# Kernel optimization log

Hardware: AMD Instinct MI355X
Metric: run time of the kernel (lower is better)

Reference implementation:

```python
import jax, jax.numpy as jnp
import numpy as np
from jax import lax

KERNEL = 3
NUM_ITERS = 10
SMOOTH = 1.0


def _max_pool3d(x):
    # x: (B, 1, Z, Y, X); 3x3x3 max pool, stride 1, SAME padding
    return lax.reduce_window(
        x, -jnp.inf, lax.max,
        window_dimensions=(1, 1, KERNEL, KERNEL, KERNEL),
        window_strides=(1, 1, 1, 1, 1),
        padding='SAME')


def _soft_erode(x):
    return -_max_pool3d(-x)


def _soft_dilate(x):
    return _max_pool3d(x)


def _soft_open(x):
    return _soft_dilate(_soft_erode(x))


def _soft_skeletonize(img):
    skel = jax.nn.relu(img - _soft_open(img))
    for _ in range(NUM_ITERS):
        img = _soft_erode(img)
        delta = jax.nn.relu(img - _soft_open(img))
        skel = skel + jax.nn.relu(delta - skel * delta)
    return skel


def setup_inputs() -> dict:
    key = jax.random.key(0)
    k1, k2 = jax.random.split(key)
    B, C, Z, Y, X = 2, 2, 192, 192, 192
    logits = jax.random.normal(k1, (B, C, Z, Y, X), dtype=jnp.float32)
    targets = jax.random.randint(k2, (B, Z, Y, X), 0, 2, dtype=jnp.int32)
    return {"logits": logits, "targets": targets}


def reference(logits, targets):
    probs = jax.nn.softmax(logits, axis=1)
    pred_surface = probs[:, 1:2]                                  # (B,1,Z,Y,X)
    gt_surface = (targets == 1).astype(jnp.float32)[:, None]      # (B,1,Z,Y,X)
    skel_pred = _soft_skeletonize(pred_surface)
    skel_gt = _soft_skeletonize(gt_surface)
    tprec = (jnp.sum(skel_pred * gt_surface) + SMOOTH) / (jnp.sum(skel_pred) + SMOOTH)
    tsens = (jnp.sum(skel_gt * pred_surface) + SMOOTH) / (jnp.sum(skel_gt) + SMOOTH)
    cl_dice = 2.0 * tprec * tsens / (tprec + tsens + 1e-07)
    return 1.0 - cl_dice
```

## Files before the change

kernel.cpp:

```cpp
#include <hip/hip_runtime.h>
#include <hip/hip_fp16.h>


#define ZD 192
#define YD 192
#define XD 192
constexpr int PLANE = YD * XD;
constexpr int VOL   = ZD * PLANE;
constexpr int NVOL4 = 4 * VOL;

constexpr int XT = 64, YT = 16, ZCH = 16;

constexpr int AWQ = 18, SA_Q = 19, AH = 22;
constexpr int NAQ = AH * AWQ;
constexpr int EWQ = 17, SE_Q = 17;
constexpr int E1H = 20;
constexpr int NE1Q = E1H * EWQ;
constexpr int E2H = 18;
constexpr int NE2Q = E2H * EWQ;
constexpr int F2STEPS = ZCH + 8;
constexpr int SAW2 = SA_Q * 2;
constexpr int SEW2 = SE_Q * 2;

constexpr int IWQ = 18, SIW = 19;
constexpr int IH  = 20;
constexpr int NIMGQ = IH * IWQ;
constexpr int BWQ = 17, BH = 18;
constexpr int NBQ  = BH * BWQ;
constexpr int TSTEPS = ZCH + 4;
#define PINF __builtin_inff()

typedef _Float16 hv2 __attribute__((ext_vector_type(2)));
struct __align__(8) H4 { hv2 lo, hi; };

__device__ __forceinline__ unsigned h2u(hv2 h) { return __builtin_bit_cast(unsigned, h); }
__device__ __forceinline__ hv2 u2h(unsigned u) { return __builtin_bit_cast(hv2, u); }

__device__ __forceinline__ hv2 h2min(hv2 a, hv2 b) {
#if __has_builtin(__builtin_elementwise_min)
    return __builtin_elementwise_min(a, b);
#else
    unsigned r, ua = h2u(a), ub = h2u(b);
    asm("v_pk_min_f16 %0, %1, %2" : "=v"(r) : "v"(ua), "v"(ub));
    return u2h(r);
#endif
}
__device__ __forceinline__ hv2 h2max(hv2 a, hv2 b) {
#if __has_builtin(__builtin_elementwise_max)
    return __builtin_elementwise_max(a, b);
#else
    unsigned r, ua = h2u(a), ub = h2u(b);
    asm("v_pk_max_f16 %0, %1, %2" : "=v"(r) : "v"(ua), "v"(ub));
    return u2h(r);
#endif
}
__device__ __forceinline__ hv2 shf1(hv2 c, hv2 n) {
    return u2h(__builtin_amdgcn_alignbit(h2u(n), h2u(c), 16));
}
__device__ __forceinline__ H4 h4min(H4 a, H4 b) { H4 r; r.lo = h2min(a.lo, b.lo); r.hi = h2min(a.hi, b.hi); return r; }
__device__ __forceinline__ H4 h4max(H4 a, H4 b) { H4 r; r.lo = h2max(a.lo, b.lo); r.hi = h2max(a.hi, b.hi); return r; }
__device__ __forceinline__ H4 pk4(float4 v) {
    H4 r;
    r.lo.x = (_Float16)v.x; r.lo.y = (_Float16)v.y;
    r.hi.x = (_Float16)v.z; r.hi.y = (_Float16)v.w;
    return r;
}
__device__ __forceinline__ H4 ldp4(const __half* p) {
    const uint2 v = *(const uint2*)p;
    H4 r; r.lo = u2h(v.x); r.hi = u2h(v.y); return r;
}
__device__ __forceinline__ void stp4(__half* p, H4 v) {
    uint2 u; u.x = h2u(v.lo); u.y = h2u(v.hi);
    *(uint2*)p = u;
}
__device__ __forceinline__ void sth4(__half* p, float4 v) { stp4(p, pk4(v)); }

template <int MODE>
__global__ __launch_bounds__(256)
void fused2p_kernel(const __half* __restrict__ a_in,
                    __half* __restrict__ a_out,
                    __half* __restrict__ skel,
                    const float* __restrict__ logits,
                    const int* __restrict__ targets)
{
    __shared__ __align__(16) hv2 sA [AH  * SA_Q * 2];
    __shared__ __align__(16) hv2 sE1[E1H * SE_Q * 2 + 2];
    __shared__ __align__(16) hv2 sE2[E2H * SE_Q * 2];

    const int tx = threadIdx.x, ty = threadIdx.y;
    const int tid = ty * 16 + tx;
    const int x0 = (blockIdx.x % 3) * XT, y0 = (blockIdx.x / 3) * YT;
    const int z0 = blockIdx.y * ZCH;
    const int zf = blockIdx.z;
    const int bb = zf & 1, field = zf >> 1;
    const size_t voff = (size_t)zf * VOL;
    const __half* inb  = a_in  + voff;
    __half*       outb = a_out + voff;
    __half*       skb  = skel  + voff;
    const float* lg0 = logits + (size_t)(bb * 2) * VOL;
    const float* lg1 = lg0 + VOL;
    const int*   tgb = targets + (size_t)bb * VOL;

    const hv2 INF2  = u2h(0x7C007C00u);
    const hv2 NINF2 = u2h(0xFC00FC00u);
    const hv2 Z2    = u2h(0u);
    const H4 HINF4  = { INF2, INF2 };
    const H4 HNINF4 = { NINF2, NINF2 };
    const H4 HZ4    = { Z2, Z2 };
    const _Float16 HN1 = (_Float16)(-PINF);

    const int q1off = ((tid & 3) << 6) + (tid >> 2);

    int a_ad[2], a_go[2]; bool a_ok[2], a_h[2];
    #pragma unroll
    for (int j = 0; j < 2; ++j) {
        const int qi = (j == 0) ? tid : 256 + q1off;
        const int r = qi / AWQ, c = qi - r * AWQ;
        const int gy = y0 - 3 + r, gxb = x0 - 4 + 4 * c;
        a_h[j]  = (qi < NAQ);
        a_ok[j] = a_h[j] && gy >= 0 && gy < YD && gxb >= 0 && gxb < XD;
        a_go[j] = gy * XD + gxb;
        a_ad[j] = (r * SA_Q + c) * 2;
    }
    int e1st[2], e1rd[2]; bool e1h[2]; H4 e1m[2];
    #pragma unroll
    for (int j = 0; j < 2; ++j) {
        const int qi = (j == 0) ? tid : 256 + q1off;
        const int r = qi / EWQ, c = qi - r * EWQ;
        e1h[j]  = (qi < NE1Q);
        e1st[j] = (r * SE_Q + c) * 2;
        e1rd[j] = (r * SA_Q + c) * 2;
        const int gy = y0 - 2 + r, gxb = x0 - 2 + 4 * c;
        const bool yv = (gy >= 0 && gy < YD);
        float4 m;
        m.x = (yv && gxb     >= 0 && gxb     < XD) ? -PINF : PINF;
        m.y = (yv && gxb + 1 >= 0 && gxb + 1 < XD) ? -PINF : PINF;
        m.z = (yv && gxb + 2 >= 0 && gxb + 2 < XD) ? -PINF : PINF;
        m.w = (yv && gxb + 3 >= 0 && gxb + 3 < XD) ? -PINF : PINF;
        e1m[j] = pk4(m);
    }
    int e2st[2], e2rd[2]; bool e2h[2]; H4 e2m[2];
    #pragma unroll
    for (int j = 0; j < 2; ++j) {
        const int qi = (j == 0) ? tid : 256 + q1off;
        const int r = qi / EWQ, c = qi - r * EWQ;
        e2h[j]  = (qi < NE2Q);
        e2st[j] = (r * SE_Q + c) * 2;
        e2rd[j] = (r * SE_Q + c) * 2;
        const int gy = y0 - 1 + r, gxb = x0 - 1 + 4 * c;
        const bool yv = (gy >= 0 && gy < YD);
        float4 m;
        m.x = (yv && gxb     >= 0 && gxb     < XD) ? PINF : -PINF;
        m.y = (yv && gxb + 1 >= 0 && gxb + 1 < XD) ? PINF : -PINF;
        m.z = (yv && gxb + 2 >= 0 && gxb + 2 < XD) ? PINF : -PINF;
        m.w = (yv && gxb + 3 >= 0 && gxb + 3 < XD) ? PINF : -PINF;
        e2m[j] = pk4(m);
    }

    const int gy0 = y0 + ty, gx0 = x0 + 4 * tx;
    const bool rok0 = (gy0 > 0), rok2 = (gy0 < YD - 1);
    const bool lok  = (gx0 > 0), rokx = (gx0 + 4 < XD);

    auto loadq = [&](int zi, int j) -> H4 {
        if (zi < 0 || zi >= ZD || zi > z0 + ZCH + 2 || !a_ok[j]) return HINF4;
        const size_t p = (size_t)zi * PLANE + a_go[j];
        if constexpr (MODE == 0) {
            if (field) {
                const int4 t = *(const int4*)(tgb + p);
                return pk4(make_float4(t.x == 1 ? 1.f : 0.f, t.y == 1 ? 1.f : 0.f,
                                       t.z == 1 ? 1.f : 0.f, t.w == 1 ? 1.f : 0.f));
            } else {
                const float4 a = *(const float4*)(lg0 + p);
                const float4 b = *(const float4*)(lg1 + p);
                return pk4(make_float4(1.f / (1.f + __expf(a.x - b.x)),
                                       1.f / (1.f + __expf(a.y - b.y)),
                                       1.f / (1.f + __expf(a.z - b.z)),
                                       1.f / (1.f + __expf(a.w - b.w))));
            }
        } else {
            return ldp4(inb + p);
        }
    };

    auto s1p = [&](int j) -> H4 {
        const hv2* p = sA + e1rd[j];
        const H4 A0 = *(const H4*)p;
        const H4 B0 = *(const H4*)(p + 2);
        const H4 A1 = *(const H4*)(p + SAW2);
        const H4 B1 = *(const H4*)(p + SAW2 + 2);
        const H4 A2 = *(const H4*)(p + 2 * SAW2);
        const H4 B2 = *(const H4*)(p + 2 * SAW2 + 2);
        const hv2 Al = h2min(A0.lo, h2min(A1.lo, A2.lo));
        const hv2 Ah = h2min(A0.hi, h2min(A1.hi, A2.hi));
        const hv2 Bl = h2min(B0.lo, h2min(B1.lo, B2.lo));
        const hv2 Bh = h2min(B0.hi, h2min(B1.hi, B2.hi));
        const hv2 M1 = shf1(Al, Ah);
        const hv2 M2 = shf1(Ah, Bl);
        const hv2 M3 = shf1(Bl, Bh);
        H4 r;
        r.lo = h2min(M1, h2min(Ah, M2));
        r.hi = h2min(M2, h2min(Bl, M3));
        return r;
    };
    auto s2p = [&](int j) -> H4 {
        const hv2* p = sE1 + e2rd[j];
        const H4 E0 = *(const H4*)p;
        const hv2 F0 = p[2];
        const H4 E1 = *(const H4*)(p + SEW2);
        const hv2 F1 = p[SEW2 + 2];
        const H4 E2 = *(const H4*)(p + 2 * SEW2);
        const hv2 F2 = p[2 * SEW2 + 2];
        const hv2 El = h2min(E0.lo, h2min(E1.lo, E2.lo));
        const hv2 Eh = h2min(E0.hi, h2min(E1.hi, E2.hi));
        const hv2 Fl = h2min(F0, h2min(F1, F2));
        const hv2 M1 = shf1(El, Eh);
        const hv2 M2 = shf1(Eh, Fl);
        H4 r;
        r.lo = h2min(El, h2min(M1, Eh));
        r.hi = h2min(Eh, h2min(M2, Fl));
        return r;
    };

    H4 s1p2a = HINF4, s1p1a = HINF4, s1p2b = HINF4, s1p1b = HINF4;
    H4 s2p2a = HINF4, s2p1a = HINF4, s2p2b = HINF4, s2p1b = HINF4;
    H4 xm1p2 = HNINF4, xm1p1 = HNINF4;
    H4 xm2p2 = HNINF4, xm2p1 = HNINF4;
    H4 e1w0 = HINF4, e1w1 = HINF4, e2w0 = HINF4, e2w1 = HINF4;
    H4 icp1 = HZ4, icp2 = HZ4, icp3 = HZ4;
    H4 ec1 = HZ4, ec2 = HZ4, ec3 = HZ4;
    H4 e2cp = HZ4;
    H4 dl1r1 = HZ4, dl1r2 = HZ4;

    const size_t eb = (size_t)gy0 * XD + gx0;

    H4 ca0 = loadq(z0 - 3, 0);
    H4 ca1 = loadq(z0 - 3, 1);

    #pragma unroll 1
    for (int s = 0; s < F2STEPS; ++s) {
        const int z = z0 - 3 + s;
        *(H4*)&sA[a_ad[0]] = ca0;
        if (a_h[1]) *(H4*)&sA[a_ad[1]] = ca1;
        if (s >= 1) {
            *(H4*)&sE1[e1st[0]] = h4max(e1w0, e1m[0]);
            if (e1h[1]) *(H4*)&sE1[e1st[1]] = h4max(e1w1, e1m[1]);
        }
        if (s >= 2) {
            *(H4*)&sE2[e2st[0]] = h4min(e2w0, e2m[0]);
            if (e2h[1]) *(H4*)&sE2[e2st[1]] = h4min(e2w1, e2m[1]);
        }
        __syncthreads();

        if (s + 1 < F2STEPS) { ca0 = loadq(z + 1, 0); ca1 = loadq(z + 1, 1); }

        {
            const H4 cur = s1p(0);
            e1w0 = h4min(s1p2a, h4min(s1p1a, cur));
            s1p2a = s1p1a; s1p1a = cur;
        }
        if (e1h[1]) {
            const H4 cur = s1p(1);
            e1w1 = h4min(s1p2b, h4min(s1p1b, cur));
            s1p2b = s1p1b; s1p1b = cur;
        }

        const int  ze1 = z - 2;
        const bool ve1 = (s >= 1) && (ze1 >= 0) && (ze1 < ZD);

        {
            const H4 cur = ve1 ? s2p(0) : HINF4;
            e2w0 = h4min(s2p2a, h4min(s2p1a, cur));
            s2p2a = s2p1a; s2p1a = cur;
        }
        if (e2h[1]) {
            const H4 cur = ve1 ? s2p(1) : HINF4;
            e2w1 = h4min(s2p2b, h4min(s2p1b, cur));
            s2p2b = s2p1b; s2p1b = cur;
        }

        H4 xm1c = HNINF4, e1cc = HZ4;
        if (ve1) {
            const hv2* p = sE1 + ((ty + 1) * SE_Q + tx) * 2;
            H4 A0 = *(const H4*)p;
            H4 Bq0 = *(const H4*)(p + 2);
            const H4 A1 = *(const H4*)(p + SEW2);
            const H4 Bq1 = *(const H4*)(p + SEW2 + 2);
            H4 A2 = *(const H4*)(p + 2 * SEW2);
            H4 Bq2 = *(const H4*)(p + 2 * SEW2 + 2);
            e1cc.lo = A1.hi;
            e1cc.hi = Bq1.lo;
            if (!rok0) { A0 = HNINF4; Bq0 = HNINF4; }
            if (!rok2) { A2 = HNINF4; Bq2 = HNINF4; }
            const hv2 Al = h2max(A0.lo, h2max(A1.lo, A2.lo));
            const hv2 Ah = h2max(A0.hi, h2max(A1.hi, A2.hi));
            const hv2 Bl = h2max(Bq0.lo, h2max(Bq1.lo, Bq2.lo));
            const hv2 Bh = h2max(Bq0.hi, h2max(Bq1.hi, Bq2.hi));
            hv2 M1 = shf1(Al, Ah);
            const hv2 M2 = shf1(Ah, Bl);
            hv2 M3 = shf1(Bl, Bh);
            if (!lok)  M1.x = HN1;
            if (!rokx) M3.y = HN1;
            xm1c.lo = h2max(M1, h2max(Ah, M2));
            xm1c.hi = h2max(M2, h2max(Bl, M3));
        }
        const H4 d1v = h4max(xm1p2, h4max(xm1p1, xm1c));
        xm1p2 = xm1p1; xm1p1 = xm1c;

        const int  ze2 = z - 4;
        const bool ve2 = (s >= 2) && (ze2 >= 0) && (ze2 < ZD);
        H4 xm2c = HNINF4, e2cc = HZ4;
        if (ve2) {
            const hv2* p = sE2 + (ty * SE_Q + tx) * 2;
            const H4 U0 = *(const H4*)p;
            const hv2 V0 = p[2];
            const H4 U1 = *(const H4*)(p + SEW2);
            const hv2 V1 = p[SEW2 + 2];
            const H4 U2 = *(const H4*)(p + 2 * SEW2);
            const hv2 V2 = p[2 * SEW2 + 2];
            e2cc.lo = shf1(U1.lo, U1.hi);
            e2cc.hi = shf1(U1.hi, V1);
            const hv2 Ul = h2max(U0.lo, h2max(U1.lo, U2.lo));
            const hv2 Uh = h2max(U0.hi, h2max(U1.hi, U2.hi));
            const hv2 Vl = h2max(V0, h2max(V1, V2));
            const hv2 M1 = shf1(Ul, Uh);
            const hv2 M2 = shf1(Uh, Vl);
            xm2c.lo = h2max(Ul, h2max(M1, Uh));
            xm2c.hi = h2max(Uh, h2max(M2, Vl));
        }
        const H4 d2v = h4max(xm2p2, h4max(xm2p1, xm2c));
        xm2p2 = xm2p1; xm2p1 = xm2c;

        const H4 icq = *(const H4*)&sA[((ty + 3) * SA_Q + tx + 1) * 2];

        float4 dl1n, dl2;
        dl1n.x = fmaxf((float)icp3.lo.x - (float)d1v.lo.x, 0.f);
        dl1n.y = fmaxf((float)icp3.lo.y - (float)d1v.lo.y, 0.f);
        dl1n.z = fmaxf((float)icp3.hi.x - (float)d1v.hi.x, 0.f);
        dl1n.w = fmaxf((float)icp3.hi.y - (float)d1v.hi.y, 0.f);
        dl2.x = fmaxf((float)ec3.lo.x - (float)d2v.lo.x, 0.f);
        dl2.y = fmaxf((float)ec3.lo.y - (float)d2v.lo.y, 0.f);
        dl2.z = fmaxf((float)ec3.hi.x - (float)d2v.hi.x, 0.f);
        dl2.w = fmaxf((float)ec3.hi.y - (float)d2v.hi.y, 0.f);
        const H4 dA = dl1r2;
        const H4 av = e2cp;

        __syncthreads();

        if (s >= 8) {
            const int zo = z - 5;
            const size_t idx = (size_t)zo * PLANE + eb;
            float4 sk;
            const float dAx = (float)dA.lo.x, dAy = (float)dA.lo.y;
            const float dAz = (float)dA.hi.x, dAw = (float)dA.hi.y;
            if constexpr (MODE == 0) {
                sk = make_float4(dAx, dAy, dAz, dAw);
            } else {
                const H4 s0 = ldp4(skb + idx);
                const float s0x = (float)s0.lo.x, s0y = (float)s0.lo.y;
                const float s0z = (float)s0.hi.x, s0w = (float)s0.hi.y;
                sk.x = s0x + dAx * (1.f - s0x);
                sk.y = s0y + dAy * (1.f - s0y);
                sk.z = s0z + dAz * (1.f - s0z);
                sk.w = s0w + dAw * (1.f - s0w);
            }
            float4 sv;
            sv.x = sk.x + dl2.x * (1.f - sk.x);
            sv.y = sk.y + dl2.y * (1.f - sk.y);
            sv.z = sk.z + dl2.z * (1.f - sk.z);
            sv.w = sk.w + dl2.w * (1.f - sk.w);
            sth4(skb + idx, sv);
            stp4(outb + idx, av);
        }

        dl1r2 = dl1r1; dl1r1 = pk4(dl1n);
        icp3 = icp2; icp2 = icp1; icp1 = icq;
        ec3 = ec2; ec2 = ec1; ec1 = e1cc;
        e2cp = e2cc;
    }
}

template <int MODE>
__global__ __launch_bounds__(256)
void fused_kernel(const __half* __restrict__ a_in,
                  __half* __restrict__ a_out,
                  __half* __restrict__ skel,
                  const float* __restrict__ logits,
                  const int* __restrict__ targets,
                  float* __restrict__ sums)
{
    __shared__ __align__(16) hv2 simg[2][IH * SIW * 2];
    __shared__ __align__(16) hv2 sbp[NBQ * 2 + 4];
    __shared__ float red[4][2];

    const int tx = threadIdx.x, ty = threadIdx.y;
    const int tid = ty * 16 + tx;
    const int x0 = (blockIdx.x % 3) * XT, y0 = (blockIdx.x / 3) * YT;
    const int z0 = blockIdx.y * ZCH;
    const int zf = blockIdx.z;
    const int bb = zf & 1, field = zf >> 1;
    const size_t voff = (size_t)zf * VOL;
    const __half* inb  = a_in  + voff;
    __half*       skb  = skel  + voff;
    const float* lg0 = logits + (size_t)(bb * 2) * VOL;
    const float* lg1 = lg0 + VOL;
    const int*   tgb = targets + (size_t)bb * VOL;

    const hv2 INF2  = u2h(0x7C007C00u);
    const hv2 NINF2 = u2h(0xFC00FC00u);
    const hv2 Z2    = u2h(0u);
    const H4 HINF4  = { INF2, INF2 };
    const H4 HNINF4 = { NINF2, NINF2 };
    const H4 HZ4    = { Z2, Z2 };

    const int q1off = ((tid & 3) << 6) + (tid >> 2);

    int im_qi[2] = { tid, 256 + q1off };
    int im_addr[2], im_goff[2]; bool im_ok[2], im_has[2];
    #pragma unroll
    for (int j = 0; j < 2; ++j) {
        const int qi = im_qi[j];
        const int r = qi / IWQ, c = qi - r * IWQ;
        const int gy = y0 - 2 + r, gxb = x0 - 4 + 4 * c;
        im_has[j] = (qi < NIMGQ);
        im_ok[j]  = im_has[j] && gy >= 0 && gy < YD && gxb >= 0 && gxb < XD;
        im_goff[j] = gy * XD + gxb;
        im_addr[j] = (r * SIW + c) * 2;
    }
    int bqi[2], brow[2], bcol[2]; bool bhas[2]; H4 bmask[2];
    #pragma unroll
    for (int j = 0; j < 2; ++j) {
        const int qi = (j == 0) ? tid : 256 + q1off;
        bqi[j] = qi;
        bhas[j] = (qi < NBQ);
        const int r = qi / BWQ, c = qi - r * BWQ;
        brow[j] = r; bcol[j] = c;
        const int gy = y0 - 1 + r, gxb = x0 - 1 + 4 * c;
        const bool yv = (gy >= 0 && gy < YD);
        float4 m;
        m.x = (yv && gxb     >= 0 && gxb     < XD) ? PINF : -PINF;
        m.y = (yv && gxb + 1 >= 0 && gxb + 1 < XD) ? PINF : -PINF;
        m.z = (yv && gxb + 2 >= 0 && gxb + 2 < XD) ? PINF : -PINF;
        m.w = (yv && gxb + 3 >= 0 && gxb + 3 < XD) ? PINF : -PINF;
        bmask[j] = pk4(m);
    }

    auto loadq = [&](int zi, int j) -> H4 {
        if (zi < 0 || zi >= ZD || !im_ok[j]) return HINF4;
        const size_t p = (size_t)zi * PLANE + im_goff[j];
        return ldp4(inb + p);
    };

    auto s1_of = [&](const hv2* sp, int j) -> H4 {
        const hv2* p = sp + (brow[j] * SIW + bcol[j]) * 2;
        const hv2 A0 = p[1];
        const hv2 A1 = p[SIW * 2 + 1];
        const hv2 A2 = p[SIW * 4 + 1];
        const H4 B0 = *(const H4*)(p + 2);
        const H4 B1 = *(const H4*)(p + SIW * 2 + 2);
        const H4 B2 = *(const H4*)(p + SIW * 4 + 2);
        const hv2 Ah = h2min(A0, h2min(A1, A2));
        const hv2 Bl = h2min(B0.lo, h2min(B1.lo, B2.lo));
        const hv2 Bh = h2min(B0.hi, h2min(B1.hi, B2.hi));
        const hv2 S1 = shf1(Ah, Bl);
        const hv2 S2 = shf1(Bl, Bh);
        H4 r;
        r.lo = h2min(Ah, h2min(S1, Bl));
        r.hi = h2min(Bl, h2min(S2, Bh));
        return r;
    };

    H4 p2a = HINF4, p1a = HINF4;
    H4 p2b = HINF4, p1b = HINF4;
    H4 s2p1 = HNINF4, s2p2 = HNINF4;
    H4 icp1 = HZ4, icp2 = HZ4;
    float sd = 0.f, ss = 0.f;

    H4 ca0 = loadq(z0 - 2, 0);
    H4 ca1 = loadq(z0 - 2, 1);

    #pragma unroll 2
    for (int s = 0; s < TSTEPS; ++s) {
        const int zi = z0 - 2 + s;
        hv2* sp = simg[s & 1];
        *(H4*)&sp[im_addr[0]] = ca0;
        if (im_has[1]) *(H4*)&sp[im_addr[1]] = ca1;
        if (s + 1 < TSTEPS) { ca0 = loadq(zi + 1, 0); ca1 = loadq(zi + 1, 1); }
        __syncthreads();
        const int zb = zi - 1;
        const bool zbv = (s >= 2) && (zb >= 0) && (zb < ZD);
        {
            const H4 cur = s1_of(sp, 0);
            if (zbv) {
                const H4 b = h4min(h4min(p2a, p1a), cur);
                *(H4*)&sbp[2 * bqi[0]] = h4min(b, bmask[0]);
            }
            p2a = p1a; p1a = cur;
        }
        if (bhas[1]) {
            const H4 cur = s1_of(sp, 1);
            if (zbv) {
                const H4 b = h4min(h4min(p2b, p1b), cur);
                *(H4*)&sbp[2 * bqi[1]] = h4min(b, bmask[1]);
            }
            p2b = p1b; p1b = cur;
        }
        const H4 icq = *(const H4*)&sp[((ty + 2) * SIW + tx + 1) * 2];
        __syncthreads();
        H4 s2n = HNINF4;
        if (zbv) {
            const hv2* p = sbp + (ty * BWQ + tx) * 2;
            const H4 U0 = *(const H4*)p;
            const H4 U1 = *(const H4*)(p + BWQ * 2);
            const H4 U2 = *(const H4*)(p + BWQ * 4);
            const hv2 V0 = p[2];
            const hv2 V1 = p[BWQ * 2 + 2];
            const hv2 V2 = p[BWQ * 4 + 2];
            const hv2 Ul = h2max(U0.lo, h2max(U1.lo, U2.lo));
            const hv2 Uh = h2max(U0.hi, h2max(U1.hi, U2.hi));
            const hv2 Vl = h2max(V0, h2max(V1, V2));
            const hv2 S1 = shf1(Ul, Uh);
            const hv2 S2 = shf1(Uh, Vl);
            s2n.lo = h2max(Ul, h2max(S1, Uh));
            s2n.hi = h2max(Uh, h2max(S2, Vl));
        }
        if (s >= 4) {
            const int zo = zi - 2;
            const H4 d = h4max(s2p2, h4max(s2p1, s2n));
            float4 dl;
            dl.x = fmaxf((float)icp2.lo.x - (float)d.lo.x, 0.f);
            dl.y = fmaxf((float)icp2.lo.y - (float)d.lo.y, 0.f);
            dl.z = fmaxf((float)icp2.hi.x - (float)d.hi.x, 0.f);
            dl.w = fmaxf((float)icp2.hi.y - (float)d.hi.y, 0.f);
            const size_t idx = (size_t)zo * PLANE + (size_t)(y0 + ty) * XD + (x0 + 4 * tx);
            const H4 sk = ldp4(skb + idx);
            const float s0x = (float)sk.lo.x, s0y = (float)sk.lo.y;
            const float s0z = (float)sk.hi.x, s0w = (float)sk.hi.y;
            float4 sv;
            sv.x = s0x + dl.x * (1.f - s0x);
            sv.y = s0y + dl.y * (1.f - s0y);
            sv.z = s0z + dl.z * (1.f - s0z);
            sv.w = s0w + dl.w * (1.f - s0w);
            float4 w;
            if (field) {
                const float4 a = *(const float4*)(lg0 + idx);
                const float4 b = *(const float4*)(lg1 + idx);
                w = make_float4(1.f / (1.f + __expf(a.x - b.x)),
                                1.f / (1.f + __expf(a.y - b.y)),
                                1.f / (1.f + __expf(a.z - b.z)),
                                1.f / (1.f + __expf(a.w - b.w)));
            } else {
                const int4 t = *(const int4*)(tgb + idx);
                w = make_float4(t.x == 1 ? 1.f : 0.f, t.y == 1 ? 1.f : 0.f,
                                t.z == 1 ? 1.f : 0.f, t.w == 1 ? 1.f : 0.f);
            }
            sd += sv.x * w.x + sv.y * w.y + sv.z * w.z + sv.w * w.w;
            ss += sv.x + sv.y + sv.z + sv.w;
        }
        s2p2 = s2p1; s2p1 = s2n;
        icp2 = icp1; icp1 = icq;
    }

    if constexpr (MODE == 2) {
        #pragma unroll
        for (int o = 32; o; o >>= 1) {
            sd += __shfl_down(sd, o, 64);
            ss += __shfl_down(ss, o, 64);
        }
        const int w = tid >> 6;
        if ((tid & 63) == 0) { red[w][0] = sd; red[w][1] = ss; }
        __syncthreads();
        if (tid == 0) {
            float a = 0.f, b = 0.f;
            #pragma unroll
            for (int i = 0; i < 4; ++i) { a += red[i][0]; b += red[i][1]; }
            atomicAdd(&sums[2 * field + 0], a);
            atomicAdd(&sums[2 * field + 1], b);
        }
    }
}

__global__ void final_kernel(const float* __restrict__ sums, float* __restrict__ out)
{
    float tprec = (sums[0] + 1.f) / (sums[1] + 1.f);
    float tsens = (sums[2] + 1.f) / (sums[3] + 1.f);
    float cl = 2.f * tprec * tsens / (tprec + tsens + 1e-7f);
    out[0] = 1.f - cl;
}

extern "C" void kernel_launch(void* const* d_in, const int* in_sizes, int n_in,
                              void* d_out, int out_size, void* d_ws, size_t ws_size,
                              hipStream_t stream)
{
    const float* logits  = (const float*)d_in[0];
    const int*   targets = (const int*)d_in[1];
    float* out  = (float*)d_out;

    float*  sums = (float*)d_ws;
    __half* A    = (__half*)(sums + 16);
    __half* B    = A + NVOL4;
    __half* SK   = B + NVOL4;

    hipMemsetAsync(sums, 0, 16 * sizeof(float), stream);

    dim3 g(3 * (YD / YT), ZD / ZCH, 4);
    dim3 blk(16, 16, 1);

    fused2p_kernel<0><<<g, blk, 0, stream>>>(A, A, SK, logits, targets);
    fused2p_kernel<1><<<g, blk, 0, stream>>>(A, B, SK, logits, targets);
    fused2p_kernel<1><<<g, blk, 0, stream>>>(B, A, SK, logits, targets);
    fused2p_kernel<1><<<g, blk, 0, stream>>>(A, B, SK, logits, targets);
    fused2p_kernel<1><<<g, blk, 0, stream>>>(B, A, SK, logits, targets);
    fused_kernel<2><<<g, blk, 0, stream>>>(A, B, SK, logits, targets, sums);

    final_kernel<<<1, 1, 0, stream>>>(sums, out);
}
```

Baseline: 919.5 us.

## Double-buffer shared plane buffers and drop the second per-step barrier

Gives the sA, sE1 and sE2 shared-memory staging buffers two copies that alternate by step parity. With this, each step writes into one buffer while other threads may still read the previous one, so the trailing __syncthreads per z-step is removed. The loop is also unrolled by two so the buffer selection can become constant. This doubles LDS usage per block, which may lower occupancy, and correctness depends on no reads spanning more than one step.

```diff
diff --git a/kernel.cpp b/kernel.cpp
--- a/kernel.cpp
+++ b/kernel.cpp
@@ -83,9 +83,9 @@
                     const float* __restrict__ logits,
                     const int* __restrict__ targets)
 {
-    __shared__ __align__(16) hv2 sA [AH  * SA_Q * 2];
-    __shared__ __align__(16) hv2 sE1[E1H * SE_Q * 2 + 2];
-    __shared__ __align__(16) hv2 sE2[E2H * SE_Q * 2];
+    __shared__ __align__(16) hv2 sA [2][AH  * SA_Q * 2];
+    __shared__ __align__(16) hv2 sE1[2][E1H * SE_Q * 2 + 2];
+    __shared__ __align__(16) hv2 sE2[2][E2H * SE_Q * 2];
 
     const int tx = threadIdx.x, ty = threadIdx.y;
     const int tid = ty * 16 + tx;
@@ -182,8 +182,8 @@
         }
     };
 
-    auto s1p = [&](int j) -> H4 {
-        const hv2* p = sA + e1rd[j];
+    auto s1p = [&](const hv2* pA, int j) -> H4 {
+        const hv2* p = pA + e1rd[j];
         const H4 A0 = *(const H4*)p;
         const H4 B0 = *(const H4*)(p + 2);
         const H4 A1 = *(const H4*)(p + SAW2);
@@ -202,8 +202,8 @@
         r.hi = h2min(M2, h2min(Bl, M3));
         return r;
     };
-    auto s2p = [&](int j) -> H4 {
-        const hv2* p = sE1 + e2rd[j];
+    auto s2p = [&](const hv2* pE1, int j) -> H4 {
+        const hv2* p = pE1 + e2rd[j];
         const H4 E0 = *(const H4*)p;
         const hv2 F0 = p[2];
         const H4 E1 = *(const H4*)(p + SEW2);
@@ -236,30 +236,33 @@
     H4 ca0 = loadq(z0 - 3, 0);
     H4 ca1 = loadq(z0 - 3, 1);
 
-    #pragma unroll 1
+    #pragma unroll 2
     for (int s = 0; s < F2STEPS; ++s) {
         const int z = z0 - 3 + s;
-        *(H4*)&sA[a_ad[0]] = ca0;
-        if (a_h[1]) *(H4*)&sA[a_ad[1]] = ca1;
+        hv2* pA  = sA [s & 1];
+        hv2* pE1 = sE1[s & 1];
+        hv2* pE2 = sE2[s & 1];
+        *(H4*)&pA[a_ad[0]] = ca0;
+        if (a_h[1]) *(H4*)&pA[a_ad[1]] = ca1;
         if (s >= 1) {
-            *(H4*)&sE1[e1st[0]] = h4max(e1w0, e1m[0]);
-            if (e1h[1]) *(H4*)&sE1[e1st[1]] = h4max(e1w1, e1m[1]);
+            *(H4*)&pE1[e1st[0]] = h4max(e1w0, e1m[0]);
+            if (e1h[1]) *(H4*)&pE1[e1st[1]] = h4max(e1w1, e1m[1]);
         }
         if (s >= 2) {
-            *(H4*)&sE2[e2st[0]] = h4min(e2w0, e2m[0]);
-            if (e2h[1]) *(H4*)&sE2[e2st[1]] = h4min(e2w1, e2m[1]);
+            *(H4*)&pE2[e2st[0]] = h4min(e2w0, e2m[0]);
+            if (e2h[1]) *(H4*)&pE2[e2st[1]] = h4min(e2w1, e2m[1]);
         }
         __syncthreads();
 
         if (s + 1 < F2STEPS) { ca0 = loadq(z + 1, 0); ca1 = loadq(z + 1, 1); }
 
         {
-            const H4 cur = s1p(0);
+            const H4 cur = s1p(pA, 0);
             e1w0 = h4min(s1p2a, h4min(s1p1a, cur));
             s1p2a = s1p1a; s1p1a = cur;
         }
         if (e1h[1]) {
-            const H4 cur = s1p(1);
+            const H4 cur = s1p(pA, 1);
             e1w1 = h4min(s1p2b, h4min(s1p1b, cur));
             s1p2b = s1p1b; s1p1b = cur;
         }
@@ -268,19 +271,19 @@
         const bool ve1 = (s >= 1) && (ze1 >= 0) && (ze1 < ZD);
 
         {
-            const H4 cur = ve1 ? s2p(0) : HINF4;
+            const H4 cur = ve1 ? s2p(pE1, 0) : HINF4;
             e2w0 = h4min(s2p2a, h4min(s2p1a, cur));
             s2p2a = s2p1a; s2p1a = cur;
         }
         if (e2h[1]) {
-            const H4 cur = ve1 ? s2p(1) : HINF4;
+            const H4 cur = ve1 ? s2p(pE1, 1) : HINF4;
             e2w1 = h4min(s2p2b, h4min(s2p1b, cur));
             s2p2b = s2p1b; s2p1b = cur;
         }
 
         H4 xm1c = HNINF4, e1cc = HZ4;
         if (ve1) {
-            const hv2* p = sE1 + ((ty + 1) * SE_Q + tx) * 2;
+            const hv2* p = pE1 + ((ty + 1) * SE_Q + tx) * 2;
             H4 A0 = *(const H4*)p;
             H4 Bq0 = *(const H4*)(p + 2);
             const H4 A1 = *(const H4*)(p + SEW2);
@@ -310,7 +313,7 @@
         const bool ve2 = (s >= 2) && (ze2 >= 0) && (ze2 < ZD);
         H4 xm2c = HNINF4, e2cc = HZ4;
         if (ve2) {
-            const hv2* p = sE2 + (ty * SE_Q + tx) * 2;
+            const hv2* p = pE2 + (ty * SE_Q + tx) * 2;
             const H4 U0 = *(const H4*)p;
             const hv2 V0 = p[2];
             const H4 U1 = *(const H4*)(p + SEW2);
@@ -330,7 +333,7 @@
         const H4 d2v = h4max(xm2p2, h4max(xm2p1, xm2c));
         xm2p2 = xm2p1; xm2p1 = xm2c;
 
-        const H4 icq = *(const H4*)&sA[((ty + 3) * SA_Q + tx + 1) * 2];
+        const H4 icq = *(const H4*)&pA[((ty + 3) * SA_Q + tx + 1) * 2];
 
         float4 dl1n, dl2;
         dl1n.x = fmaxf((float)icp3.lo.x - (float)d1v.lo.x, 0.f);
@@ -343,8 +346,6 @@
         dl2.w = fmaxf((float)ec3.hi.y - (float)d2v.hi.y, 0.f);
         const H4 dA = dl1r2;
         const H4 av = e2cp;
-
-        __syncthreads();
 
         if (s >= 8) {
             const int zo = z - 5;
```

New measurement: 938.2 us. 1.02x slower.
